# Performance work log

Hardware: AMD Instinct MI355X
Metric: run time of the kernel (lower is better)

## Reference

```python
import jax, jax.numpy as jnp
import numpy as np

N_SITES, NODE_F = 50000, 64
N_PERM, N_NEIGH = 12, 8
IN_F = N_NEIGH * NODE_F  # 512
OUT_F = 64
LN2 = float(np.log(2.0))


def setup_inputs() -> dict:
    key = jax.random.key(0)
    k1, k2, k3, k4 = jax.random.split(key, 4)
    X_sites = jax.random.normal(k1, (N_SITES, NODE_F), dtype=jnp.float32)
    X_NSs = jax.random.randint(k2, (N_SITES, N_PERM, N_NEIGH), 0, N_SITES)
    # nn.Linear(IN_F, OUT_F): weight (OUT_F, IN_F), bias (OUT_F,)
    bound = 1.0 / np.sqrt(IN_F)
    W = jax.random.uniform(k3, (OUT_F, IN_F), minval=-bound, maxval=bound, dtype=jnp.float32)
    b = jax.random.uniform(k4, (OUT_F,), minval=-bound, maxval=bound, dtype=jnp.float32)
    return {"X_sites": X_sites, "X_NSs": X_NSs, "W": W, "b": b}


def reference(X_sites, X_NSs, W, b):
    # Gather neighbor features: (N, P, K, F) -> (N, P, K*F)
    gathered = X_sites[X_NSs].reshape(X_NSs.shape[0], N_PERM, IN_F)
    # Linear: (N, P, IN_F) @ (IN_F, OUT_F) + b
    x1 = jnp.einsum('npi,oi->npo', gathered, W) + b
    # Shifted softplus: softplus(x) - log(2)  (dropout treated as identity / eval mode)
    x2 = jax.nn.softplus(x1) - LN2
    # Sum over permutations -> (N, OUT_F)
    return x2.sum(axis=1)
```

## Files before the change

### kernel.cpp

```cpp
#include <hip/hip_runtime.h>
#include <hip/hip_bf16.h>

#define N_SITES 50000
#define N_PERM  12
#define N_NEIGH 8
#define NODE_F  64
#define IN_F    512
#define OUT_F   64
#define N_TILES (N_SITES / 16)
#define LN2F    0.69314718055994530942f

#define XCHUNKS (N_SITES * NODE_F / 8)
#define WCHUNKS (OUT_F * IN_F / 8)
#define SLOT_E  520
#define BUF_E   (16 * SLOT_E)

typedef __bf16 bf16x8 __attribute__((ext_vector_type(8)));
typedef float  f32x4  __attribute__((ext_vector_type(4)));

__device__ __forceinline__ unsigned short f32_to_bf16_rne(unsigned int u) {
    u += 0x7FFFu + ((u >> 16) & 1u);
    return (unsigned short)(u >> 16);
}

__device__ __forceinline__ int probe_is_bf16(const void* Xorig) {
    int lane = threadIdx.x & 63;
    unsigned short h = ((const unsigned short*)Xorig)[2 * lane];
    int e = (h >> 7) & 0xFF;
    unsigned long long mm = __ballot(e >= 110 && e <= 140);
    return (__popcll(mm) >= 48) ? 1 : 0;
}

__device__ __forceinline__ void pack8(const uint4* src, uint4* dst, int c) {
    uint4 a = src[2 * c], b = src[2 * c + 1];
    uint4 o;
    o.x = (unsigned int)f32_to_bf16_rne(a.x) | ((unsigned int)f32_to_bf16_rne(a.y) << 16);
    o.y = (unsigned int)f32_to_bf16_rne(a.z) | ((unsigned int)f32_to_bf16_rne(a.w) << 16);
    o.z = (unsigned int)f32_to_bf16_rne(b.x) | ((unsigned int)f32_to_bf16_rne(b.y) << 16);
    o.w = (unsigned int)f32_to_bf16_rne(b.z) | ((unsigned int)f32_to_bf16_rne(b.w) << 16);
    dst[c] = o;
}

__global__ void convert_all(const void* __restrict__ Xv, const void* __restrict__ Wv,
                            const void* __restrict__ Bv, uint4* __restrict__ Xb,
                            uint4* __restrict__ Wb, float* __restrict__ Bf) {
    const int isbf = probe_is_bf16(Xv);
    int c = blockIdx.x * blockDim.x + threadIdx.x;
    if (c < XCHUNKS) {
        if (isbf) Xb[c] = ((const uint4*)Xv)[c];
        else      pack8((const uint4*)Xv, Xb, c);
    } else if (c < XCHUNKS + WCHUNKS) {
        int cw = c - XCHUNKS;
        if (isbf) Wb[cw] = ((const uint4*)Wv)[cw];
        else      pack8((const uint4*)Wv, Wb, cw);
    } else if (c < XCHUNKS + WCHUNKS + OUT_F) {
        int i = c - XCHUNKS - WCHUNKS;
        Bf[i] = isbf ? (float)((const __bf16*)Bv)[i] : ((const float*)Bv)[i];
    }
}

__device__ __forceinline__ float softplus_sh(float x) {
    float t = __expf(-fabsf(x));
    return fmaxf(x, 0.f) + 0.69314718056f * __log2f(1.f + t);
}

__device__ __forceinline__ void async16(const __bf16* g, __bf16* l) {
    __builtin_amdgcn_global_load_lds(
        (const __attribute__((address_space(1))) unsigned int*)g,
        (__attribute__((address_space(3))) unsigned int*)l, 16, 0, 0);
}

__global__ __launch_bounds__(256, 2)
void lcnn_dma(const void* __restrict__ Xorig, const __bf16* __restrict__ Xb,
              const int* __restrict__ NS, const __bf16* __restrict__ Wb,
              const float* __restrict__ Bf, void* __restrict__ outv)
{
    __shared__ __align__(16) __bf16 Abuf[2][BUF_E];

    const int wave = threadIdx.x >> 6;
    const int lane = threadIdx.x & 63;
    const int m    = lane & 15;
    const int quad = lane >> 4;
    const int mk   = m & 7;
    const int mh   = m >> 3;
    const int tile = blockIdx.x;

    bf16x8 Wfrag[16];
    #pragma unroll
    for (int ks = 0; ks < 16; ++ks)
        Wfrag[ks] = *(const bf16x8*)(Wb + (size_t)(wave * 16 + m) * IN_F + ks * 32 + quad * 8);

    const float bias = Bf[wave * 16 + m];

    auto load_idx = [&](int p_, int out[4]) {
        #pragma unroll
        for (int i = 0; i < 4; ++i) {
            int t = wave * 4 + i;
            int s = ((t & 1) << 3) + (lane >> 3);
            int k = t >> 1;
            out[i] = NS[(size_t)(tile * 16 + s) * (N_PERM * N_NEIGH) + p_ * N_NEIGH + k];
        }
    };
    auto stage = [&](int buf_, const int idxv[4]) {
        const int csrc = (lane & 7) ^ (lane >> 3);
        #pragma unroll
        for (int i = 0; i < 4; ++i) {
            int t = wave * 4 + i;
            async16(Xb + (size_t)idxv[i] * NODE_F + csrc * 8, &Abuf[buf_][t * SLOT_E]);
        }
    };

    int idxn[4];
    load_idx(0, idxn);
    stage(0, idxn);
    load_idx(1, idxn);
    __syncthreads();

    f32x4 sum = {0.f, 0.f, 0.f, 0.f};
    for (int p = 0; p < N_PERM; ++p) {
        if (p < N_PERM - 1) stage((p + 1) & 1, idxn);
        if (p < N_PERM - 2) load_idx(p + 2, idxn);

        f32x4 acc = {0.f, 0.f, 0.f, 0.f};
        const __bf16* bb = &Abuf[p & 1][0];
        #pragma unroll
        for (int ks = 0; ks < 16; ++ks) {
            int t_r = (ks >> 1) * 2 + mh;
            int j   = ((ks & 1) << 2) | quad;
            bf16x8 afr = *(const bf16x8*)(bb + t_r * SLOT_E + mk * 64 + ((j ^ mk) << 3));
            acc = __builtin_amdgcn_mfma_f32_16x16x32_bf16(afr, Wfrag[ks], acc, 0, 0, 0);
        }
        #pragma unroll
        for (int r = 0; r < 4; ++r) sum[r] += softplus_sh(acc[r] + bias);
        __syncthreads();
    }

    const int isbf = probe_is_bf16(Xorig);
    #pragma unroll
    for (int r = 0; r < 4; ++r) {
        size_t pos = (size_t)(tile * 16 + quad * 4 + r) * OUT_F + wave * 16 + m;
        float v = sum[r] - 12.0f * LN2F;
        if (isbf) ((__bf16*)outv)[pos] = (__bf16)v;
        else      ((float*)outv)[pos]  = v;
    }
}

__global__ void lcnn_fallback(const float* __restrict__ X, const int* __restrict__ NS,
                              const float* __restrict__ W, const float* __restrict__ B,
                              float* __restrict__ out) {
    int t = blockIdx.x * blockDim.x + threadIdx.x;
    if (t >= N_SITES * OUT_F) return;
    int sitei = t >> 6, o = t & 63;
    const int* ns = NS + (size_t)sitei * 96;
    float s = 0.f;
    for (int p = 0; p < N_PERM; ++p) {
        float x = B[o];
        for (int n = 0; n < N_NEIGH; ++n) {
            const float* xr = X + (size_t)ns[p * 8 + n] * NODE_F;
            const float* wr = W + (size_t)o * IN_F + n * NODE_F;
            for (int f = 0; f < NODE_F; ++f) x += xr[f] * wr[f];
        }
        s += softplus_sh(x);
    }
    out[t] = s - 12.0f * LN2F;
}

extern "C" void kernel_launch(void* const* d_in, const int* in_sizes, int n_in,
                              void* d_out, int out_size, void* d_ws, size_t ws_size,
                              hipStream_t stream) {
    const void* X  = d_in[0];
    const int*  NS = (const int*)d_in[1];
    const void* W  = d_in[2];
    const void* B  = d_in[3];

    char* ws = (char*)d_ws;
    __bf16* Xb = (__bf16*)ws;
    __bf16* Wb = (__bf16*)(ws + (size_t)XCHUNKS * 16);
    float*  Bf = (float*)(ws + (size_t)(XCHUNKS + WCHUNKS) * 16);
    const bool conv = ws_size >= (size_t)(XCHUNKS + WCHUNKS) * 16 + OUT_F * 4;

    if (conv) {
        int nch = XCHUNKS + WCHUNKS + OUT_F;
        hipLaunchKernelGGL(convert_all, dim3((nch + 255) / 256), dim3(256), 0, stream,
                           X, W, B, (uint4*)Xb, (uint4*)Wb, Bf);
        hipLaunchKernelGGL(lcnn_dma, dim3(N_TILES), dim3(256), 0, stream,
                           X, Xb, NS, Wb, Bf, d_out);
    } else {
        hipLaunchKernelGGL(lcnn_fallback,
                           dim3((N_SITES * OUT_F + 255) / 256), dim3(256), 0, stream,
                           (const float*)X, NS, (const float*)W, (const float*)B,
                           (float*)d_out);
    }
}
```

Baseline: 144.3 us.

## Halve waves per block, each wave computes two 16-column output tiles

Shrinks the main kernel from four waves to two per block. Each wave now holds weight fragments for two 16-wide output slices and issues two MFMAs per A fragment read from LDS. Each wave also stages eight gathered rows per permutation instead of four. This halves LDS A-fragment reads per MFMA and cuts the thread count, at the cost of doubled weight-register pressure per wave (32 bf16x8 fragments) and fewer waves to hide gather latency.

```diff
diff --git a/kernel.cpp b/kernel.cpp
--- a/kernel.cpp
+++ b/kernel.cpp
@@ -70,7 +70,7 @@
         (__attribute__((address_space(3))) unsigned int*)l, 16, 0, 0);
 }
 
-__global__ __launch_bounds__(256, 2)
+__global__ __launch_bounds__(128, 2)
 void lcnn_dma(const void* __restrict__ Xorig, const __bf16* __restrict__ Xb,
               const int* __restrict__ NS, const __bf16* __restrict__ Wb,
               const float* __restrict__ Bf, void* __restrict__ outv)
@@ -85,63 +85,77 @@
     const int mh   = m >> 3;
     const int tile = blockIdx.x;
 
-    bf16x8 Wfrag[16];
+    bf16x8 Wfrag[2][16];
     #pragma unroll
-    for (int ks = 0; ks < 16; ++ks)
-        Wfrag[ks] = *(const bf16x8*)(Wb + (size_t)(wave * 16 + m) * IN_F + ks * 32 + quad * 8);
-
-    const float bias = Bf[wave * 16 + m];
-
-    auto load_idx = [&](int p_, int out[4]) {
-        #pragma unroll
-        for (int i = 0; i < 4; ++i) {
-            int t = wave * 4 + i;
+    for (int nb = 0; nb < 2; ++nb)
+        #pragma unroll
+        for (int ks = 0; ks < 16; ++ks)
+            Wfrag[nb][ks] = *(const bf16x8*)(
+                Wb + (size_t)(wave * 32 + nb * 16 + m) * IN_F + ks * 32 + quad * 8);
+
+    const float bias0 = Bf[wave * 32 + m];
+    const float bias1 = Bf[wave * 32 + 16 + m];
+
+    auto load_idx = [&](int p_, int out[8]) {
+        #pragma unroll
+        for (int i = 0; i < 8; ++i) {
+            int t = wave * 8 + i;
             int s = ((t & 1) << 3) + (lane >> 3);
             int k = t >> 1;
             out[i] = NS[(size_t)(tile * 16 + s) * (N_PERM * N_NEIGH) + p_ * N_NEIGH + k];
         }
     };
-    auto stage = [&](int buf_, const int idxv[4]) {
+    auto stage = [&](int buf_, const int idxv[8]) {
         const int csrc = (lane & 7) ^ (lane >> 3);
         #pragma unroll
-        for (int i = 0; i < 4; ++i) {
-            int t = wave * 4 + i;
+        for (int i = 0; i < 8; ++i) {
+            int t = wave * 8 + i;
             async16(Xb + (size_t)idxv[i] * NODE_F + csrc * 8, &Abuf[buf_][t * SLOT_E]);
         }
     };
 
-    int idxn[4];
+    int idxn[8];
     load_idx(0, idxn);
     stage(0, idxn);
     load_idx(1, idxn);
     __syncthreads();
 
-    f32x4 sum = {0.f, 0.f, 0.f, 0.f};
+    f32x4 sum0 = {0.f, 0.f, 0.f, 0.f}, sum1 = {0.f, 0.f, 0.f, 0.f};
     for (int p = 0; p < N_PERM; ++p) {
         if (p < N_PERM - 1) stage((p + 1) & 1, idxn);
         if (p < N_PERM - 2) load_idx(p + 2, idxn);
 
-        f32x4 acc = {0.f, 0.f, 0.f, 0.f};
+        f32x4 acc0 = {0.f, 0.f, 0.f, 0.f}, acc1 = {0.f, 0.f, 0.f, 0.f};
         const __bf16* bb = &Abuf[p & 1][0];
         #pragma unroll
         for (int ks = 0; ks < 16; ++ks) {
             int t_r = (ks >> 1) * 2 + mh;
             int j   = ((ks & 1) << 2) | quad;
             bf16x8 afr = *(const bf16x8*)(bb + t_r * SLOT_E + mk * 64 + ((j ^ mk) << 3));
-            acc = __builtin_amdgcn_mfma_f32_16x16x32_bf16(afr, Wfrag[ks], acc, 0, 0, 0);
-        }
-        #pragma unroll
-        for (int r = 0; r < 4; ++r) sum[r] += softplus_sh(acc[r] + bias);
+            acc0 = __builtin_amdgcn_mfma_f32_16x16x32_bf16(afr, Wfrag[0][ks], acc0, 0, 0, 0);
+            acc1 = __builtin_amdgcn_mfma_f32_16x16x32_bf16(afr, Wfrag[1][ks], acc1, 0, 0, 0);
+        }
+        #pragma unroll
+        for (int r = 0; r < 4; ++r) {
+            sum0[r] += softplus_sh(acc0[r] + bias0);
+            sum1[r] += softplus_sh(acc1[r] + bias1);
+        }
         __syncthreads();
     }
 
     const int isbf = probe_is_bf16(Xorig);
     #pragma unroll
     for (int r = 0; r < 4; ++r) {
-        size_t pos = (size_t)(tile * 16 + quad * 4 + r) * OUT_F + wave * 16 + m;
-        float v = sum[r] - 12.0f * LN2F;
-        if (isbf) ((__bf16*)outv)[pos] = (__bf16)v;
-        else      ((float*)outv)[pos]  = v;
+        size_t row = (size_t)(tile * 16 + quad * 4 + r) * OUT_F;
+        float v0 = sum0[r] - 12.0f * LN2F;
+        float v1 = sum1[r] - 12.0f * LN2F;
+        if (isbf) {
+            ((__bf16*)outv)[row + wave * 32 + m]      = (__bf16)v0;
+            ((__bf16*)outv)[row + wave * 32 + 16 + m] = (__bf16)v1;
+        } else {
+            ((float*)outv)[row + wave * 32 + m]      = v0;
+            ((float*)outv)[row + wave * 32 + 16 + m] = v1;
+        }
     }
 }
 
@@ -183,7 +197,7 @@
         int nch = XCHUNKS + WCHUNKS + OUT_F;
         hipLaunchKernelGGL(convert_all, dim3((nch + 255) / 256), dim3(256), 0, stream,
                            X, W, B, (uint4*)Xb, (uint4*)Wb, Bf);
-        hipLaunchKernelGGL(lcnn_dma, dim3(N_TILES), dim3(256), 0, stream,
+        hipLaunchKernelGGL(lcnn_dma, dim3(N_TILES), dim3(128), 0, stream,
                            X, Xb, NS, Wb, Bf, d_out);
     } else {
         hipLaunchKernelGGL(lcnn_fallback,
```

Measured after the change: 155.2 us. 1.08x slower.
